# Optimization experiments

Hardware: AMD Instinct MI355X
Metric: run time of the kernel (lower is better)

The kernel has to match this reference:

```python
import jax, jax.numpy as jnp
import numpy as np

B, N, D = 8, 256, 3          # batch, particles, spatial dims
H = 64                        # hidden_nf (channels)
L = 4                         # num_layers
ENC = 3                       # atom_type, aa_type, aa_pos
IN_NF = ENC + 1               # + time
COORDS_RANGE = 15.0 / L       # tanh=True -> coords_range/n_layers
E = B * N * N                 # fully-connected edges per batch graph


def _linear(key, fin, fout):
    k1, k2 = jax.random.split(key)
    s = 1.0 / np.sqrt(fin)
    w = jax.random.uniform(k1, (fout, fin), minval=-s, maxval=s, dtype=jnp.float32)
    b = jax.random.uniform(k2, (fout,), minval=-s, maxval=s, dtype=jnp.float32)
    return w, b


def setup_inputs() -> dict:
    key = jax.random.key(0)
    ks = jax.random.split(key, 64)
    inp = {
        "t": jax.random.uniform(ks[0], (B, 1), dtype=jnp.float32),
        "x": jax.random.normal(ks[1], (B, N * D), dtype=jnp.float32),
        "atom_type": jax.random.uniform(ks[2], (B, N), dtype=jnp.float32),
        "aa_type": jax.random.uniform(ks[3], (B, N), dtype=jnp.float32),
        "aa_pos": jax.random.uniform(ks[4], (B, N), dtype=jnp.float32),
        "node_mask": jnp.ones((B, N), dtype=jnp.float32),
    }
    inp["emb_w"], inp["emb_b"] = _linear(ks[5], IN_NF, H)
    specs = [("edge_w1", "edge_b1", 2 * H + 2, H), ("edge_w2", "edge_b2", H, H),
             ("node_w1", "node_b1", 2 * H, H), ("node_w2", "node_b2", H, H),
             ("coord_w1", "coord_b1", H, H), ("att_w", "att_b", H, 1)]
    kk = 6
    for wn, bn, fin, fout in specs:
        ws, bs = [], []
        for _ in range(L):
            w, b = _linear(ks[kk], fin, fout); kk += 1
            ws.append(w); bs.append(b)
        inp[wn] = jnp.stack(ws); inp[bn] = jnp.stack(bs)
    # final coord layer: Linear(H,1,bias=False), xavier gain 0.001
    inp["coord_w2"] = jax.random.normal(ks[kk], (L, 1, H), dtype=jnp.float32) * 0.001
    return inp


def _edges():
    idx = jnp.arange(N)
    row_in = jnp.repeat(idx, N)
    col_in = jnp.tile(idx, N)
    off = (jnp.arange(B) * N)[:, None]
    row = (off + row_in[None, :]).reshape(-1)
    col = (off + col_in[None, :]).reshape(-1)
    return row, col


def reference(t, x, atom_type, aa_type, aa_pos, node_mask,
              emb_w, emb_b, edge_w1, edge_b1, edge_w2, edge_b2,
              node_w1, node_b1, node_w2, node_b2,
              coord_w1, coord_b1, att_w, att_b, coord_w2):
    silu = jax.nn.silu
    row, col = _edges()
    nm = node_mask.reshape(B * N, 1)
    # edge mask: pairwise node mask with diagonal (self-loop) removed
    em = ((node_mask[:, :, None] * node_mask[:, None, :])
          * (1.0 - jnp.eye(N, dtype=jnp.float32))).reshape(E, 1)

    x0 = x.reshape(B * N, D) * nm
    tt = jnp.broadcast_to(t, (B, N)).reshape(B * N, 1) * nm
    h = jnp.stack([atom_type, aa_type, aa_pos], axis=-1).reshape(B * N, ENC) * nm
    h = jnp.concatenate([h, tt], axis=1)                      # [BN, 4]
    edge_attr0 = jnp.sum((x0[row] - x0[col]) ** 2, axis=1, keepdims=True)  # [E,1]

    h = h @ emb_w.T + emb_b                                   # embedding -> [BN, H]
    coord = x0
    for l in range(L):
        diff = coord[row] - coord[col]                        # [E, D]
        radial = jnp.sum(diff ** 2, axis=1, keepdims=True)    # [E, 1]
        diff = diff / (jnp.sqrt(radial + 1e-8) + 1.0)         # norm_diff
        m = jnp.concatenate([h[row], h[col], radial, edge_attr0], axis=1)
        m = silu(m @ edge_w1[l].T + edge_b1[l])
        m = silu(m @ edge_w2[l].T + edge_b2[l])               # [E, H]
        m = m * jax.nn.sigmoid(m @ att_w[l].T + att_b[l]) * em
        phi = jnp.tanh(silu(m @ coord_w1[l].T + coord_b1[l]) @ coord_w2[l].T)
        trans = diff * phi * COORDS_RANGE * em                # [E, D]
        coord = (coord + jax.ops.segment_sum(trans, row, num_segments=B * N)) * nm
        agg = jax.ops.segment_sum(m, row, num_segments=B * N)  # [BN, H]
        upd = jnp.concatenate([h, agg], axis=1)
        upd = silu(upd @ node_w1[l].T + node_b1[l]) @ node_w2[l].T + node_b2[l]
        h = (h + upd) * nm                                    # recurrent residual

    vel = (coord - x0) * nm
    vel = vel.reshape(B, N, D)
    nmr = node_mask.reshape(B, N, 1)
    Ns = jnp.sum(nmr, axis=1, keepdims=True)
    vel = vel - (jnp.sum(vel, axis=1, keepdims=True) / Ns) * nmr  # remove_mean_with_mask
    return vel.reshape(B, N * D)
```

## Files before the change

kernel.cpp:

```cpp
#include <hip/hip_runtime.h>

#define CRANGE 3.75f

typedef _Float16 half_t;
typedef __attribute__((ext_vector_type(8))) _Float16 half8;
typedef __attribute__((ext_vector_type(4))) _Float16 half4;
typedef __attribute__((ext_vector_type(4))) float f32x4;

__device__ __forceinline__ float frcp(float x) { return __builtin_amdgcn_rcpf(x); }
__device__ __forceinline__ float fexpn(float x) { return __expf(fminf(x, 20.f)); }
__device__ __forceinline__ float fsilu(float x) { return x * frcp(1.f + fexpn(-x)); }

__device__ __forceinline__ void inv4(float d0, float d1, float d2, float d3, float* o) {
    float p01 = d0 * d1, p23 = d2 * d3;
    float r = frcp(p01 * p23);
    float t01 = p23 * r, t23 = p01 * r;
    o[0] = d1 * t01; o[1] = d0 * t01; o[2] = d3 * t23; o[3] = d2 * t23;
}
__device__ __forceinline__ void silu4(const float* x, float* o) {
    float d0 = 1.f + fexpn(-x[0]), d1 = 1.f + fexpn(-x[1]);
    float d2 = 1.f + fexpn(-x[2]), d3 = 1.f + fexpn(-x[3]);
    float iv[4]; inv4(d0, d1, d2, d3, iv);
    o[0] = x[0] * iv[0]; o[1] = x[1] * iv[1]; o[2] = x[2] * iv[2]; o[3] = x[3] * iv[3];
}

__global__ void k_prep(const float* __restrict__ ew2, const float* __restrict__ cw1,
                       const float* __restrict__ nw1, const float* __restrict__ nw2,
                       const float* __restrict__ ew1,
                       half_t* __restrict__ wf, float* __restrict__ trT) {
    int idx = blockIdx.x * 256 + threadIdx.x;
    if (idx < 4096) {
        int lane = idx & 63;
        int g = (idx >> 6) & 7;
        int mat = (idx >> 9) & 1;
        int l = idx >> 10;
        int mt = g >> 1, kc = g & 1;
        int c = lane & 15, qq = lane >> 4;
        const float* W = (mat ? cw1 : ew2) + l * 4096;
        int row = 16 * mt + c;
        int k0 = 32 * kc + 8 * qq;
        half8 pk;
#pragma unroll
        for (int j = 0; j < 8; ++j) pk[j] = (half_t)W[row * 64 + k0 + j];
        ((half8*)wf)[idx] = pk;
    }
    int tid2 = idx - 4096;
    if (tid2 >= 0 && tid2 < 81920) {
        int l = tid2 / 20480, r = tid2 % 20480;
        float v;
        if (r < 8192)       { int k = r >> 6,        c = r & 63; v = nw1[l * 8192 + c * 128 + k]; }
        else if (r < 12288) { int r2 = r - 8192,  k = r2 >> 6, c = r2 & 63; v = nw2[l * 4096 + c * 64 + k]; }
        else if (r < 16384) { int r2 = r - 12288, k = r2 >> 6, c = r2 & 63; v = ew1[l * 8320 + c * 130 + k]; }
        else                { int r2 = r - 16384, k = r2 >> 6, c = r2 & 63; v = ew1[l * 8320 + c * 130 + 64 + k]; }
        trT[l * 20480 + r] = v;
    }
}

__global__ void k_init(const float* __restrict__ t, const float* __restrict__ x,
                       const float* __restrict__ at, const float* __restrict__ aa,
                       const float* __restrict__ ap, const float* __restrict__ nm,
                       const float* __restrict__ embw, const float* __restrict__ embb,
                       const float* __restrict__ ew1aT0, const float* __restrict__ ew1bT0,
                       const float* __restrict__ eb1_0,
                       float* __restrict__ h, float* __restrict__ Hr, float* __restrict__ HcA,
                       float* __restrict__ x0, float* __restrict__ cA) {
    int n = blockIdx.x, c = threadIdx.x;
    __shared__ float sh[64];
    float m = nm[n]; int b = n >> 8;
    float i0 = at[n] * m, i1 = aa[n] * m, i2 = ap[n] * m, i3 = t[b] * m;
    float4 w = ((const float4*)embw)[c];
    float hv = w.x * i0 + w.y * i1 + w.z * i2 + w.w * i3 + embb[c];
    sh[c] = hv; h[n * 64 + c] = hv;
    if (c < 3) { float v = x[n * 3 + c] * m; x0[n * 3 + c] = v; cA[n * 3 + c] = v; }
    __syncthreads();
    float a = eb1_0[c], bb = 0.f;
#pragma unroll
    for (int k = 0; k < 64; ++k) {
        float hk = sh[k];
        a  += ew1aT0[k * 64 + c] * hk;
        bb += ew1bT0[k * 64 + c] * hk;
    }
    Hr[n * 64 + c] = a;
    HcA[n * 64 + c] = bb;
}

__global__ __launch_bounds__(256, 3) void k_edge(
    const float* __restrict__ coordIn, const float* __restrict__ x0,
    float* __restrict__ Hr, const float* __restrict__ Hc,
    const float* __restrict__ ew1, const float* __restrict__ eb2,
    const float* __restrict__ cb1, const float* __restrict__ attw,
    const float* __restrict__ attb, const float* __restrict__ cw2,
    const float* __restrict__ nm, const half_t* __restrict__ wf2,
    const half_t* __restrict__ wf1,
    float* __restrict__ hbuf,
    const float* __restrict__ nw1T, const float* __restrict__ nw2T,
    const float* __restrict__ nb1, const float* __restrict__ nb2,
    const float* __restrict__ ew1aTn, const float* __restrict__ ew1bTn,
    const float* __restrict__ eb1n,
    float* __restrict__ HcO, float* __restrict__ coordOut)
{
    __shared__ __align__(16) half_t sV[4][4096];
    __shared__ __align__(16) float sGeo[4][64][4];
    __shared__ float sHr[64], sWr[64], sWe[64], sB2[64], sBc1[64], sAttw[64], sWc2[64];
    __shared__ float sAgg[64];
    __shared__ float sCoord[3];

    const int i = blockIdx.x, b = i >> 8, ir = i & 255;
    const int t = threadIdx.x, wv = t >> 6, e = t & 63;
    const int q = e >> 4, c = e & 15;
    const int col = (b << 8) + t;

    if (t < 64) {
        sHr[t] = Hr[i * 64 + t];
        sWr[t] = ew1[t * 130 + 128];
        sWe[t] = ew1[t * 130 + 129];
        sB2[t] = eb2[t]; sBc1[t] = cb1[t]; sAttw[t] = attw[t]; sWc2[t] = cw2[t];
        sAgg[t] = 0.f;
    }
    if (t == 64) { sCoord[0] = 0.f; sCoord[1] = 0.f; sCoord[2] = 0.f; }
    float attb0 = attb[0];
    float nmi = nm[i];

    float dx = coordIn[i*3+0] - coordIn[col*3+0];
    float dy = coordIn[i*3+1] - coordIn[col*3+1];
    float dz = coordIn[i*3+2] - coordIn[col*3+2];
    float radial = dx*dx + dy*dy + dz*dz;
    float inv = frcp(__builtin_amdgcn_sqrtf(radial + 1e-8f) + 1.f);
    float ex = x0[i*3+0] - x0[col*3+0];
    float ey = x0[i*3+1] - x0[col*3+1];
    float ez = x0[i*3+2] - x0[col*3+2];
    float e0 = ex*ex + ey*ey + ez*ez;
    float em = nmi * nm[col] * ((t == ir) ? 0.f : 1.f);

    __syncthreads();

    {
        float4 g4 = make_float4(dx*inv, dy*inv, dz*inv, em);
        *(float4*)&sGeo[wv][e][0] = g4;
    }

    half_t* mybuf = (half_t*)sV[wv];
    const float4* hcv = (const float4*)(Hc + col * 64);
#pragma unroll
    for (int s = 0; s < 8; ++s) {
        float4 ha = hcv[2*s], hb = hcv[2*s+1];
        float z[8], so[8];
        z[0]=ha.x; z[1]=ha.y; z[2]=ha.z; z[3]=ha.w;
        z[4]=hb.x; z[5]=hb.y; z[6]=hb.z; z[7]=hb.w;
#pragma unroll
        for (int u = 0; u < 8; ++u) {
            int k = 8*s + u;
            z[u] = sHr[k] + z[u] + radial * sWr[k] + e0 * sWe[k];
        }
        silu4(z, so); silu4(z + 4, so + 4);
        half8 pk;
#pragma unroll
        for (int u = 0; u < 8; ++u) pk[u] = (half_t)so[u];
        int f = q * 2 + (s >> 2);
        *(half8*)&mybuf[f * 512 + ((s & 3) * 16 + c) * 8] = pk;
    }

    const half8* bv = (const half8*)mybuf;
    f32x4 acc[4][4];
#pragma unroll
    for (int mt = 0; mt < 4; ++mt)
#pragma unroll
        for (int nt = 0; nt < 4; ++nt)
#pragma unroll
            for (int r = 0; r < 4; ++r) acc[mt][nt][r] = 0.f;
    {
        const half8* a2v = (const half8*)wf2;
        half8 a2[8];
#pragma unroll
        for (int g = 0; g < 8; ++g) a2[g] = a2v[g * 64 + e];
#pragma unroll
        for (int nt = 0; nt < 4; ++nt) {
            half8 b0 = bv[(nt*2+0)*64 + e];
            half8 b1 = bv[(nt*2+1)*64 + e];
#pragma unroll
            for (int mt = 0; mt < 4; ++mt) {
                acc[mt][nt] = __builtin_amdgcn_mfma_f32_16x16x32_f16(a2[mt*2+0], b0, acc[mt][nt], 0, 0, 0);
                acc[mt][nt] = __builtin_amdgcn_mfma_f32_16x16x32_f16(a2[mt*2+1], b1, acc[mt][nt], 0, 0, 0);
            }
        }
    }

    half8 a1[8];
    {
        const half8* a1v = (const half8*)wf1;
#pragma unroll
        for (int g = 0; g < 8; ++g) a1[g] = a1v[g * 64 + e];
    }

    float attp[4] = {0.f, 0.f, 0.f, 0.f};
#pragma unroll
    for (int mt = 0; mt < 4; ++mt) {
        int row0 = 16*mt + 4*q;
#pragma unroll
        for (int nt = 0; nt < 4; ++nt) {
            float z[4], so[4];
#pragma unroll
            for (int r = 0; r < 4; ++r) z[r] = acc[mt][nt][r] + sB2[row0 + r];
            silu4(z, so);
#pragma unroll
            for (int r = 0; r < 4; ++r) {
                acc[mt][nt][r] = so[r];
                attp[nt] += so[r] * sAttw[row0 + r];
            }
        }
    }
#pragma unroll
    for (int nt = 0; nt < 4; ++nt) {
        float v = attp[nt];
        v += __shfl_xor(v, 16);
        v += __shfl_xor(v, 32);
        attp[nt] = v;
    }
    float scale[4];
    {
        float d0 = 1.f + fexpn(-(attp[0] + attb0));
        float d1 = 1.f + fexpn(-(attp[1] + attb0));
        float d2 = 1.f + fexpn(-(attp[2] + attb0));
        float d3 = 1.f + fexpn(-(attp[3] + attb0));
        float iv[4]; inv4(d0, d1, d2, d3, iv);
#pragma unroll
        for (int nt = 0; nt < 4; ++nt) scale[nt] = iv[nt] * sGeo[wv][16*nt + c][3];
    }

    float aggp[4][4];
#pragma unroll
    for (int mt = 0; mt < 4; ++mt)
#pragma unroll
        for (int r = 0; r < 4; ++r) aggp[mt][r] = 0.f;
#pragma unroll
    for (int mt = 0; mt < 4; ++mt) {
        int kbase = 16*mt + 4*q;
        int fof = ((kbase >> 5) * 512) + (((kbase >> 3) & 3) * 128) + (kbase & 7);
#pragma unroll
        for (int nt = 0; nt < 4; ++nt) {
            half4 pk;
#pragma unroll
            for (int r = 0; r < 4; ++r) {
                float v = acc[mt][nt][r] * scale[nt];
                aggp[mt][r] += v;
                pk[r] = (half_t)v;
            }
            *(half4*)&mybuf[nt*1024 + fof + c*8] = pk;
        }
    }

#pragma unroll
    for (int mt = 0; mt < 4; ++mt)
#pragma unroll
        for (int r = 0; r < 4; ++r) {
            float v = aggp[mt][r];
            v += __shfl_xor(v, 1); v += __shfl_xor(v, 2);
            v += __shfl_xor(v, 4); v += __shfl_xor(v, 8);
            if (c == 0) atomicAdd(&sAgg[16*mt + 4*q + r], v);
        }

    f32x4 acc2[4][4];
#pragma unroll
    for (int mt = 0; mt < 4; ++mt)
#pragma unroll
        for (int nt = 0; nt < 4; ++nt)
#pragma unroll
            for (int r = 0; r < 4; ++r) acc2[mt][nt][r] = 0.f;
#pragma unroll
    for (int nt = 0; nt < 4; ++nt) {
        half8 b0 = bv[(nt*2+0)*64 + e];
        half8 b1 = bv[(nt*2+1)*64 + e];
#pragma unroll
        for (int mt = 0; mt < 4; ++mt) {
            acc2[mt][nt] = __builtin_amdgcn_mfma_f32_16x16x32_f16(a1[mt*2+0], b0, acc2[mt][nt], 0, 0, 0);
            acc2[mt][nt] = __builtin_amdgcn_mfma_f32_16x16x32_f16(a1[mt*2+1], b1, acc2[mt][nt], 0, 0, 0);
        }
    }

    float php[4] = {0.f, 0.f, 0.f, 0.f};
#pragma unroll
    for (int mt = 0; mt < 4; ++mt) {
        int row0 = 16*mt + 4*q;
#pragma unroll
        for (int nt = 0; nt < 4; ++nt) {
            float z[4], so[4];
#pragma unroll
            for (int r = 0; r < 4; ++r) z[r] = acc2[mt][nt][r] + sBc1[row0 + r];
            silu4(z, so);
#pragma unroll
            for (int r = 0; r < 4; ++r) php[nt] += so[r] * sWc2[row0 + r];
        }
    }
#pragma unroll
    for (int nt = 0; nt < 4; ++nt) {
        float v = php[nt];
        v += __shfl_xor(v, 16);
        v += __shfl_xor(v, 32);
        php[nt] = v;
    }
    float tnh[4];
    {
        float d0 = fexpn(2.f * php[0]) + 1.f;
        float d1 = fexpn(2.f * php[1]) + 1.f;
        float d2 = fexpn(2.f * php[2]) + 1.f;
        float d3 = fexpn(2.f * php[3]) + 1.f;
        float iv[4]; inv4(d0, d1, d2, d3, iv);
#pragma unroll
        for (int nt = 0; nt < 4; ++nt) tnh[nt] = 1.f - 2.f * iv[nt];
    }
    float tx = 0.f, ty = 0.f, tz = 0.f;
#pragma unroll
    for (int nt = 0; nt < 4; ++nt) {
        float4 g4 = *(float4*)&sGeo[wv][16*nt + c][0];
        float tr = tnh[nt] * CRANGE * g4.w;
        tx += g4.x * tr; ty += g4.y * tr; tz += g4.z * tr;
    }
    tx += __shfl_xor(tx, 1); tx += __shfl_xor(tx, 2); tx += __shfl_xor(tx, 4); tx += __shfl_xor(tx, 8);
    ty += __shfl_xor(ty, 1); ty += __shfl_xor(ty, 2); ty += __shfl_xor(ty, 4); ty += __shfl_xor(ty, 8);
    tz += __shfl_xor(tz, 1); tz += __shfl_xor(tz, 2); tz += __shfl_xor(tz, 4); tz += __shfl_xor(tz, 8);
    if (e == 0) {
        atomicAdd(&sCoord[0], tx);
        atomicAdd(&sCoord[1], ty);
        atomicAdd(&sCoord[2], tz);
    }

    __syncthreads();

    float* sT   = (float*)&sV[0][0];
    float* sIn  = sT;
    float* sP   = sT + 128;
    float* sU   = sT + 384;
    float* sHn  = sT + 448;
    float* sPB  = sT + 512;

    if (t < 64) sIn[t] = hbuf[i * 64 + t];
    else if (t < 128) sIn[t] = sAgg[t - 64];
    if (t >= 128 && t < 131) {
        int d = t - 128;
        coordOut[i * 3 + d] = (coordIn[i * 3 + d] + sCoord[d]) * nmi;
    }
    __syncthreads();

    const int cc = t & 63, p = t >> 6;
    {
        float a = 0.f;
        const float* w = nw1T + (p * 32) * 64 + cc;
#pragma unroll
        for (int k = 0; k < 32; ++k) a += w[k * 64] * sIn[p * 32 + k];
        sP[p * 64 + cc] = a;
    }
    __syncthreads();
    if (t < 64) sU[t] = fsilu(sP[t] + sP[64 + t] + sP[128 + t] + sP[192 + t] + nb1[t]);
    __syncthreads();
    {
        float a = 0.f;
        const float* w = nw2T + (p * 16) * 64 + cc;
#pragma unroll
        for (int k = 0; k < 16; ++k) a += w[k * 64] * sU[p * 16 + k];
        sP[p * 64 + cc] = a;
    }
    __syncthreads();
    if (t < 64) {
        float hn = (sIn[t] + sP[t] + sP[64 + t] + sP[128 + t] + sP[192 + t] + nb2[t]) * nmi;
        hbuf[i * 64 + t] = hn;
        sHn[t] = hn;
    }
    __syncthreads();
    {
        float a = 0.f, b2 = 0.f;
        const float* wa = ew1aTn + (p * 16) * 64 + cc;
        const float* wb = ew1bTn + (p * 16) * 64 + cc;
#pragma unroll
        for (int k = 0; k < 16; ++k) {
            float hv = sHn[p * 16 + k];
            a  += wa[k * 64] * hv;
            b2 += wb[k * 64] * hv;
        }
        sP[p * 64 + cc] = a;
        sPB[p * 64 + cc] = b2;
    }
    __syncthreads();
    if (t < 64) {
        Hr[i * 64 + t]  = sP[t] + sP[64 + t] + sP[128 + t] + sP[192 + t] + eb1n[t];
        HcO[i * 64 + t] = sPB[t] + sPB[64 + t] + sPB[128 + t] + sPB[192 + t];
    }
}

__global__ void k_final(const float* __restrict__ coord, const float* __restrict__ x0,
                        const float* __restrict__ nm, float* __restrict__ out) {
    int b = blockIdx.x;
    int t = threadIdx.x;
    int i = b * 256 + t;
    int lane = t & 63;
    float m = nm[i];
    float vx = (coord[i * 3 + 0] - x0[i * 3 + 0]) * m;
    float vy = (coord[i * 3 + 1] - x0[i * 3 + 1]) * m;
    float vz = (coord[i * 3 + 2] - x0[i * 3 + 2]) * m;
    __shared__ float red[4];
    if (t < 4) red[t] = 0.f;
    __syncthreads();
    float sx = vx, sy = vy, sz = vz, sn = m;
#pragma unroll
    for (int off = 1; off < 64; off <<= 1) {
        sx += __shfl_xor(sx, off);
        sy += __shfl_xor(sy, off);
        sz += __shfl_xor(sz, off);
        sn += __shfl_xor(sn, off);
    }
    if (lane == 0) {
        atomicAdd(&red[0], sx); atomicAdd(&red[1], sy);
        atomicAdd(&red[2], sz); atomicAdd(&red[3], sn);
    }
    __syncthreads();
    float invNs = frcp(red[3]);
    out[b * 768 + t * 3 + 0] = vx - red[0] * invNs * m;
    out[b * 768 + t * 3 + 1] = vy - red[1] * invNs * m;
    out[b * 768 + t * 3 + 2] = vz - red[2] * invNs * m;
}

extern "C" void kernel_launch(void* const* d_in, const int* in_sizes, int n_in,
                              void* d_out, int out_size, void* d_ws, size_t ws_size,
                              hipStream_t stream) {
    const float* t_in    = (const float*)d_in[0];
    const float* x_in    = (const float*)d_in[1];
    const float* at_in   = (const float*)d_in[2];
    const float* aa_in   = (const float*)d_in[3];
    const float* ap_in   = (const float*)d_in[4];
    const float* nm_in   = (const float*)d_in[5];
    const float* emb_w   = (const float*)d_in[6];
    const float* emb_b   = (const float*)d_in[7];
    const float* edge_w1 = (const float*)d_in[8];
    const float* edge_b1 = (const float*)d_in[9];
    const float* edge_w2 = (const float*)d_in[10];
    const float* edge_b2 = (const float*)d_in[11];
    const float* node_w1 = (const float*)d_in[12];
    const float* node_b1 = (const float*)d_in[13];
    const float* node_w2 = (const float*)d_in[14];
    const float* node_b2 = (const float*)d_in[15];
    const float* coord_w1= (const float*)d_in[16];
    const float* coord_b1= (const float*)d_in[17];
    const float* att_w   = (const float*)d_in[18];
    const float* att_b   = (const float*)d_in[19];
    const float* coord_w2= (const float*)d_in[20];

    float* ws  = (float*)d_ws;
    float* h   = ws;
    float* Hr  = h + 131072;
    float* HcA = Hr + 131072;
    float* HcB = HcA + 131072;
    float* x0  = HcB + 131072;
    float* cA  = x0 + 6144;
    float* cB  = cA + 6144;
    float* base = cB + 6144;
    half_t* wf = (half_t*)base;
    float* trT = base + 16384;

    float* out = (float*)d_out;

    k_prep<<<336, 256, 0, stream>>>(edge_w2, coord_w1, node_w1, node_w2, edge_w1, wf, trT);
    k_init<<<2048, 64, 0, stream>>>(t_in, x_in, at_in, aa_in, ap_in, nm_in, emb_w, emb_b,
                                    trT + 12288, trT + 16384, edge_b1,
                                    h, Hr, HcA, x0, cA);

    for (int l = 0; l < 4; ++l) {
        const float* ew1 = edge_w1 + l * 8320;
        const float* eb2 = edge_b2 + l * 64;
        const float* cb1 = coord_b1 + l * 64;
        const float* aw  = att_w + l * 64;
        const float* ab  = att_b + l;
        const float* cw2 = coord_w2 + l * 64;
        const float* nb1 = node_b1 + l * 64;
        const float* nb2 = node_b2 + l * 64;

        const float* trL = trT + l * 20480;
        int ln = (l + 1) & 3;
        const float* trN = trT + ln * 20480;

        const float* cin  = (l & 1) ? cB : cA;
        float*       cout = (l & 1) ? cA : cB;
        const float* HcR  = (l & 1) ? HcB : HcA;
        float*       HcW  = (l & 1) ? HcA : HcB;

        k_edge<<<2048, 256, 0, stream>>>(cin, x0, Hr, HcR, ew1, eb2, cb1,
                                         aw, ab, cw2, nm_in,
                                         wf + l * 8192, wf + l * 8192 + 4096,
                                         h, trL, trL + 8192, nb1, nb2,
                                         trN + 12288, trN + 16384, edge_b1 + ln * 64,
                                         HcW, cout);
    }

    k_final<<<8, 256, 0, stream>>>(cA, x0, nm_in, out);
}
```

Before: 310.7 us.

## Split edge MLP GEMMs into two K-chunks to halve per-wave LDS staging

The edge kernel now produces the first-layer SiLU activations and the scaled second-layer outputs in two K-halves, running the MFMAs for each half before writing the next. This halves the per-wave shared buffer (4096 to 2048 halves per wave), cutting LDS per block, which may allow more resident blocks or ease LDS pressure. It also interleaves the MFMA work with the elementwise work. In exchange it adds extra dependency points between writes and reads of the shared buffer and may raise register pressure, since the a2 weights are loaded earlier.

```diff
diff --git a/kernel.cpp b/kernel.cpp
--- a/kernel.cpp
+++ b/kernel.cpp
@@ -99,7 +99,7 @@
     const float* __restrict__ eb1n,
     float* __restrict__ HcO, float* __restrict__ coordOut)
 {
-    __shared__ __align__(16) half_t sV[4][4096];
+    __shared__ __align__(16) half_t sV[4][2048];
     __shared__ __align__(16) float sGeo[4][64][4];
     __shared__ float sHr[64], sWr[64], sWe[64], sB2[64], sBc1[64], sAttw[64], sWc2[64];
     __shared__ float sAgg[64];
@@ -140,27 +140,16 @@
     }
 
     half_t* mybuf = (half_t*)sV[wv];
+    const half8* bv = (const half8*)mybuf;
     const float4* hcv = (const float4*)(Hc + col * 64);
-#pragma unroll
-    for (int s = 0; s < 8; ++s) {
-        float4 ha = hcv[2*s], hb = hcv[2*s+1];
-        float z[8], so[8];
-        z[0]=ha.x; z[1]=ha.y; z[2]=ha.z; z[3]=ha.w;
-        z[4]=hb.x; z[5]=hb.y; z[6]=hb.z; z[7]=hb.w;
-#pragma unroll
-        for (int u = 0; u < 8; ++u) {
-            int k = 8*s + u;
-            z[u] = sHr[k] + z[u] + radial * sWr[k] + e0 * sWe[k];
-        }
-        silu4(z, so); silu4(z + 4, so + 4);
-        half8 pk;
-#pragma unroll
-        for (int u = 0; u < 8; ++u) pk[u] = (half_t)so[u];
-        int f = q * 2 + (s >> 2);
-        *(half8*)&mybuf[f * 512 + ((s & 3) * 16 + c) * 8] = pk;
-    }
-
-    const half8* bv = (const half8*)mybuf;
+
+    half8 a2[8];
+    {
+        const half8* a2v = (const half8*)wf2;
+#pragma unroll
+        for (int g = 0; g < 8; ++g) a2[g] = a2v[g * 64 + e];
+    }
+
     f32x4 acc[4][4];
 #pragma unroll
     for (int mt = 0; mt < 4; ++mt)
@@ -168,20 +157,33 @@
         for (int nt = 0; nt < 4; ++nt)
 #pragma unroll
             for (int r = 0; r < 4; ++r) acc[mt][nt][r] = 0.f;
-    {
-        const half8* a2v = (const half8*)wf2;
-        half8 a2[8];
-#pragma unroll
-        for (int g = 0; g < 8; ++g) a2[g] = a2v[g * 64 + e];
+
+#pragma unroll
+    for (int kc = 0; kc < 2; ++kc) {
+#pragma unroll
+        for (int s2 = 0; s2 < 4; ++s2) {
+            int s = kc * 4 + s2;
+            float4 ha = hcv[2*s], hb = hcv[2*s+1];
+            float z[8], so[8];
+            z[0]=ha.x; z[1]=ha.y; z[2]=ha.z; z[3]=ha.w;
+            z[4]=hb.x; z[5]=hb.y; z[6]=hb.z; z[7]=hb.w;
+#pragma unroll
+            for (int u = 0; u < 8; ++u) {
+                int k = 8*s + u;
+                z[u] = sHr[k] + z[u] + radial * sWr[k] + e0 * sWe[k];
+            }
+            silu4(z, so); silu4(z + 4, so + 4);
+            half8 pk;
+#pragma unroll
+            for (int u = 0; u < 8; ++u) pk[u] = (half_t)so[u];
+            *(half8*)&mybuf[q * 512 + (s2 * 16 + c) * 8] = pk;
+        }
 #pragma unroll
         for (int nt = 0; nt < 4; ++nt) {
-            half8 b0 = bv[(nt*2+0)*64 + e];
-            half8 b1 = bv[(nt*2+1)*64 + e];
-#pragma unroll
-            for (int mt = 0; mt < 4; ++mt) {
-                acc[mt][nt] = __builtin_amdgcn_mfma_f32_16x16x32_f16(a2[mt*2+0], b0, acc[mt][nt], 0, 0, 0);
-                acc[mt][nt] = __builtin_amdgcn_mfma_f32_16x16x32_f16(a2[mt*2+1], b1, acc[mt][nt], 0, 0, 0);
-            }
+            half8 b0 = bv[nt * 64 + e];
+#pragma unroll
+            for (int mt = 0; mt < 4; ++mt)
+                acc[mt][nt] = __builtin_amdgcn_mfma_f32_16x16x32_f16(a2[mt*2+kc], b0, acc[mt][nt], 0, 0, 0);
         }
     }
 
@@ -232,20 +234,40 @@
     for (int mt = 0; mt < 4; ++mt)
 #pragma unroll
         for (int r = 0; r < 4; ++r) aggp[mt][r] = 0.f;
-#pragma unroll
-    for (int mt = 0; mt < 4; ++mt) {
-        int kbase = 16*mt + 4*q;
-        int fof = ((kbase >> 5) * 512) + (((kbase >> 3) & 3) * 128) + (kbase & 7);
+
+    f32x4 acc2[4][4];
+#pragma unroll
+    for (int mt = 0; mt < 4; ++mt)
+#pragma unroll
+        for (int nt = 0; nt < 4; ++nt)
+#pragma unroll
+            for (int r = 0; r < 4; ++r) acc2[mt][nt][r] = 0.f;
+
+#pragma unroll
+    for (int kc = 0; kc < 2; ++kc) {
+#pragma unroll
+        for (int mi = 0; mi < 2; ++mi) {
+            int mt = kc * 2 + mi;
+            int kbase = 16*mt + 4*q;
+            int off = (((kbase >> 3) & 3) * 128) + (kbase & 7) + c * 8;
+#pragma unroll
+            for (int nt = 0; nt < 4; ++nt) {
+                half4 pk;
+#pragma unroll
+                for (int r = 0; r < 4; ++r) {
+                    float v = acc[mt][nt][r] * scale[nt];
+                    aggp[mt][r] += v;
+                    pk[r] = (half_t)v;
+                }
+                *(half4*)&mybuf[nt * 512 + off] = pk;
+            }
+        }
 #pragma unroll
         for (int nt = 0; nt < 4; ++nt) {
-            half4 pk;
-#pragma unroll
-            for (int r = 0; r < 4; ++r) {
-                float v = acc[mt][nt][r] * scale[nt];
-                aggp[mt][r] += v;
-                pk[r] = (half_t)v;
-            }
-            *(half4*)&mybuf[nt*1024 + fof + c*8] = pk;
+            half8 b0 = bv[nt * 64 + e];
+#pragma unroll
+            for (int mt = 0; mt < 4; ++mt)
+                acc2[mt][nt] = __builtin_amdgcn_mfma_f32_16x16x32_f16(a1[mt*2+kc], b0, acc2[mt][nt], 0, 0, 0);
         }
     }
 
@@ -258,24 +280,6 @@
             v += __shfl_xor(v, 4); v += __shfl_xor(v, 8);
             if (c == 0) atomicAdd(&sAgg[16*mt + 4*q + r], v);
         }
-
-    f32x4 acc2[4][4];
-#pragma unroll
-    for (int mt = 0; mt < 4; ++mt)
-#pragma unroll
-        for (int nt = 0; nt < 4; ++nt)
-#pragma unroll
-            for (int r = 0; r < 4; ++r) acc2[mt][nt][r] = 0.f;
-#pragma unroll
-    for (int nt = 0; nt < 4; ++nt) {
-        half8 b0 = bv[(nt*2+0)*64 + e];
-        half8 b1 = bv[(nt*2+1)*64 + e];
-#pragma unroll
-        for (int mt = 0; mt < 4; ++mt) {
-            acc2[mt][nt] = __builtin_amdgcn_mfma_f32_16x16x32_f16(a1[mt*2+0], b0, acc2[mt][nt], 0, 0, 0);
-            acc2[mt][nt] = __builtin_amdgcn_mfma_f32_16x16x32_f16(a1[mt*2+1], b1, acc2[mt][nt], 0, 0, 0);
-        }
-    }
 
     float php[4] = {0.f, 0.f, 0.f, 0.f};
 #pragma unroll
```

Measured after the change: 352.8 us. 13.5% more time.
